# Kernel tuning notes

Hardware: AMD Instinct MI355X
Metric: run time of the kernel (lower is better)

Reference implementation:

```python
import jax, jax.numpy as jnp
import numpy as np

B, T, D, H, QK = 4, 2048, 1024, 16, 64
MAX_WAVELENGTH = 10000


def apply_rope(x, positions):
    # x: [B, T, H, d]; positions: [B, T] int
    d = x.shape[-1]
    fraction = 2 * jnp.arange(0, d // 2, dtype=jnp.int32) / d
    timescale = MAX_WAVELENGTH ** fraction  # [d/2]
    sinusoid = positions[..., None] / timescale[None, :]  # [B, T, d/2]
    sinusoid = sinusoid[..., None, :]  # [B, T, 1, d/2]
    sin, cos = jnp.sin(sinusoid), jnp.cos(sinusoid)
    x1, x2 = jnp.split(x, 2, axis=-1)
    return jnp.concatenate([x1 * cos - x2 * sin, x2 * cos + x1 * sin], axis=-1).astype(x.dtype)


def rms_norm(x, scale):
    var = jnp.mean(jnp.square(x), axis=-1, keepdims=True)
    return x * jax.lax.rsqrt(var + 1e-6) * (1 + scale)


def setup_inputs() -> dict:
    key = jax.random.key(0)
    ks = jax.random.split(key, 12)
    s = 0.02
    pos = jnp.broadcast_to(jnp.arange(T, dtype=jnp.int32), (B, T))
    causal = jnp.tril(jnp.ones((T, T), dtype=bool))[None, None]  # [1,1,T,T]
    return {
        "q": jax.random.normal(ks[0], (B, T, D), jnp.float32),
        "kv": jax.random.normal(ks[1], (B, T, D), jnp.float32),
        "mask": jnp.broadcast_to(causal, (B, 1, T, T)),
        "q_positions": pos,
        "kv_positions": pos,
        "Wq": jax.random.normal(ks[2], (D, H * QK), jnp.float32) * s,
        "bq": jnp.zeros((H * QK,), jnp.float32),
        "Wk": jax.random.normal(ks[3], (D, H * QK), jnp.float32) * s,
        "bk": jnp.zeros((H * QK,), jnp.float32),
        "Wv": jax.random.normal(ks[4], (D, H * QK), jnp.float32) * s,
        "bv": jnp.zeros((H * QK,), jnp.float32),
        "q_scale": jnp.zeros((QK,), jnp.float32),
        "k_scale": jnp.zeros((QK,), jnp.float32),
        "head_scale": jnp.zeros((1, H, 1), jnp.float32),
        "Wo": jax.random.normal(ks[5], (H * QK, D), jnp.float32) * s,
        "bo": jnp.zeros((D,), jnp.float32),
    }


def reference(q, kv, mask, q_positions, kv_positions, Wq, bq, Wk, bk, Wv, bv,
              q_scale, k_scale, head_scale, Wo, bo):
    qh = (q @ Wq + bq).reshape(B, T, H, QK)
    kh = (kv @ Wk + bk).reshape(B, T, H, QK)
    vh = (kv @ Wv + bv).reshape(B, T, H, QK)
    # qk layer norm (RMSNorm with (1+scale))
    qh = rms_norm(qh, q_scale)
    kh = rms_norm(kh, k_scale)
    # RoPE
    qh = apply_rope(qh, q_positions)
    kh = apply_rope(kh, kv_positions)
    # attention
    logits = jnp.einsum('bthd,bThd->bhtT', qh, kh) / np.sqrt(QK).astype(q.dtype)
    logits = jnp.where(mask, logits, jnp.finfo(logits.dtype).min)
    weights = jax.nn.softmax(logits, axis=-1)
    weights = jnp.where(mask, weights, 0)
    attn = jnp.einsum('bhtT,bThd->bthd', weights, vh)
    attn = attn * (1 + head_scale)  # [1,H,1] broadcasts over (t,h,d)
    return attn.reshape(B, T, H * QK) @ Wo + bo
```

## Files before the change

### kernel.cpp

```cpp
#include <hip/hip_runtime.h>
#include <math.h>

#define BB 4
#define TT 2048
#define DD 1024
#define HH 16
#define QKD 64
#define MM (BB*TT)
#define NN 1024
#define KK 1024

typedef unsigned short u16;
typedef __attribute__((ext_vector_type(8))) short short8;
typedef __attribute__((ext_vector_type(4))) float float4v;

__device__ __forceinline__ u16 f2bf(float f) {
    union { float f; unsigned u; } v; v.f = f;
    unsigned r = (v.u + 0x7FFFu + ((v.u >> 16) & 1u)) >> 16;
    return (u16)r;
}

typedef __attribute__((address_space(3))) unsigned lds_u32_t;
typedef __attribute__((address_space(1))) const unsigned glb_u32_t;
__device__ __forceinline__ void gl2lds16(const u16* g, u16* l) {
    __builtin_amdgcn_global_load_lds((glb_u32_t*)g, (lds_u32_t*)l, 16, 0, 0);
}

__global__ __launch_bounds__(256) void acast_kernel(
    const float* __restrict__ a, const float* __restrict__ b,
    u16* __restrict__ da, u16* __restrict__ db)
{
    const float* s = blockIdx.y ? b : a;
    u16* d = blockIdx.y ? db : da;
    size_t i = ((size_t)blockIdx.x * 256 + threadIdx.x) * 4;
    float4 v = *(const float4*)&s[i];
    ushort4 o = { f2bf(v.x), f2bf(v.y), f2bf(v.z), f2bf(v.w) };
    *(ushort4*)&d[i] = o;
}

__global__ __launch_bounds__(256) void wt_kernel(
    const float* __restrict__ Wq, const float* __restrict__ Wk,
    const float* __restrict__ Wv, const float* __restrict__ Wo,
    u16* __restrict__ dstbase)
{
    const int z = blockIdx.z;
    const float* src = (z == 0) ? Wq : (z == 1) ? Wk : (z == 2) ? Wv : Wo;
    u16* out = dstbase + (size_t)z * (KK * NN);
    const int bi = blockIdx.y, bj = blockIdx.x;
    __shared__ float tile[64][65];
    const int t = threadIdx.x;
    #pragma unroll
    for (int p = 0; p < 4; p++) {
        int idx = p * 256 + t;
        int r = idx >> 4, c4 = (idx & 15) << 2;
        float4 v = *(const float4*)&src[(size_t)(bi * 64 + r) * NN + bj * 64 + c4];
        tile[r][c4 + 0] = v.x; tile[r][c4 + 1] = v.y;
        tile[r][c4 + 2] = v.z; tile[r][c4 + 3] = v.w;
    }
    __syncthreads();
    #pragma unroll
    for (int p = 0; p < 4; p++) {
        int idx = p * 256 + t;
        int rn = idx >> 4, c4 = (idx & 15) << 2;
        ushort4 o = { f2bf(tile[c4 + 0][rn]), f2bf(tile[c4 + 1][rn]),
                      f2bf(tile[c4 + 2][rn]), f2bf(tile[c4 + 3][rn]) };
        *(ushort4*)&out[(size_t)(bj * 64 + rn) * KK + bi * 64 + c4] = o;
    }
}

__device__ __forceinline__ void gemm_mainloop(
    const u16* __restrict__ A, const u16* __restrict__ Bt,
    int m0, int n0, u16* As, u16* Bs, float4v (&acc)[4][4])
{
    const int tid = threadIdx.x;
    const int wave = tid >> 6, lane = tid & 63;
    const int l15 = lane & 15, lg = lane >> 4;
    const int wm = wave >> 1, wn = wave & 1;

    const int lr = lane >> 3;
    const int lc = lane & 7;

    for (int k0 = 0; k0 < KK; k0 += 64) {
        #pragma unroll
        for (int i = 0; i < 4; i++) {
            int chunk = wave * 4 + i;
            int row = chunk * 8 + lr;
            int gcb = lc ^ (row & 7);
            gl2lds16(A  + (size_t)(m0 + row) * KK + k0 + gcb * 8, As + chunk * 512);
            gl2lds16(Bt + (size_t)(n0 + row) * KK + k0 + gcb * 8, Bs + chunk * 512);
        }
        __syncthreads();

        short8 af[2][4], bf[2][4];
        #pragma unroll
        for (int kc = 0; kc < 2; kc++) {
            #pragma unroll
            for (int x = 0; x < 4; x++) {
                int ra = wm * 64 + x * 16 + l15;
                int sa = (kc * 4 + lg) ^ (ra & 7);
                af[kc][x] = *(const short8*)(As + ra * 64 + sa * 8);
                int rb = wn * 64 + x * 16 + l15;
                int sb = (kc * 4 + lg) ^ (rb & 7);
                bf[kc][x] = *(const short8*)(Bs + rb * 64 + sb * 8);
            }
        }
        #pragma unroll
        for (int mi = 0; mi < 4; mi++)
            #pragma unroll
            for (int nj = 0; nj < 4; nj++) {
                acc[mi][nj] = __builtin_amdgcn_mfma_f32_16x16x32_bf16(af[0][mi], bf[0][nj], acc[mi][nj], 0, 0, 0);
                acc[mi][nj] = __builtin_amdgcn_mfma_f32_16x16x32_bf16(af[1][mi], bf[1][nj], acc[mi][nj], 0, 0, 0);
            }
        __syncthreads();
    }
}

__global__ __launch_bounds__(256) void qkv_gemm(
    const u16* __restrict__ qb, const u16* __restrict__ kvb,
    const u16* __restrict__ Wt,
    const float* __restrict__ bq, const float* __restrict__ bk, const float* __restrict__ bv,
    const int* __restrict__ qpos, const int* __restrict__ kpos,
    const float* __restrict__ q_scale, const float* __restrict__ k_scale,
    u16* __restrict__ qh, u16* __restrict__ kh, u16* __restrict__ vh)
{
    __shared__ u16 As[128 * 64];
    __shared__ u16 Bs[128 * 64];

    const int z = blockIdx.z;
    const u16* A        = (z == 0) ? qb : kvb;
    const u16* B        = Wt + (size_t)z * (KK * NN);
    const float* bias   = (z == 0) ? bq : (z == 1) ? bk : bv;
    const float* scl    = (z == 0) ? q_scale : k_scale;
    const int* pos_arr  = (z == 0) ? qpos : kpos;
    u16* dst            = (z == 0) ? qh : (z == 1) ? kh : vh;

    const int m0 = blockIdx.y * 128, n0 = blockIdx.x * 128;

    float4v acc[4][4];
    #pragma unroll
    for (int i = 0; i < 4; i++)
        #pragma unroll
        for (int j = 0; j < 4; j++) acc[i][j] = (float4v){0.f, 0.f, 0.f, 0.f};

    gemm_mainloop(A, B, m0, n0, As, Bs, acc);

    const int lane = threadIdx.x & 63, wave = threadIdx.x >> 6;
    const int l15 = lane & 15, lg = lane >> 4;
    const int wm = wave >> 1, wn = wave & 1;
    const int mbase = m0 + wm * 64;
    const int nbase = n0 + wn * 64;
    const int h = nbase >> 6;

    float bia[4], sc[4];
    #pragma unroll
    for (int nj = 0; nj < 4; nj++) {
        bia[nj] = bias[nbase - (h << 6) + h * 64 + nj * 16 + l15];
        sc[nj]  = 1.0f + scl[nj * 16 + l15];
    }
    float invts[2];
    #pragma unroll
    for (int p = 0; p < 2; p++)
        invts[p] = powf(10000.0f, -(float)(p * 16 + l15) * (1.0f / 32.0f));

    const float QMUL = 0.125f * 1.44269504088896340736f;

    #pragma unroll
    for (int mi = 0; mi < 4; mi++) {
        #pragma unroll
        for (int r = 0; r < 4; r++) {
            const int m = mbase + mi * 16 + lg * 4 + r;
            const int b = m >> 11, t = m & 2047;
            float v[4];
            #pragma unroll
            for (int nj = 0; nj < 4; nj++) v[nj] = acc[mi][nj][r] + bia[nj];

            if (z < 2) {
                float ss = v[0]*v[0] + v[1]*v[1] + v[2]*v[2] + v[3]*v[3];
                ss += __shfl_xor(ss, 1);
                ss += __shfl_xor(ss, 2);
                ss += __shfl_xor(ss, 4);
                ss += __shfl_xor(ss, 8);
                float rn = rsqrtf(ss * (1.0f / 64.0f) + 1e-6f);
                #pragma unroll
                for (int nj = 0; nj < 4; nj++) v[nj] = v[nj] * rn * sc[nj];

                const float pos = (float)pos_arr[b * TT + t];
                #pragma unroll
                for (int p = 0; p < 2; p++) {
                    float ang = pos * invts[p];
                    float s = sinf(ang), c = cosf(ang);
                    float x1 = v[p], x2 = v[p + 2];
                    v[p]     = x1 * c - x2 * s;
                    v[p + 2] = x2 * c + x1 * s;
                }
                if (z == 0) {
                    #pragma unroll
                    for (int nj = 0; nj < 4; nj++) v[nj] *= QMUL;
                }
            }
            u16* op = dst + ((size_t)((b * HH + h) * TT + t)) * QKD + l15;
            #pragma unroll
            for (int nj = 0; nj < 4; nj++) op[nj * 16] = f2bf(v[nj]);
        }
    }
}

__global__ __launch_bounds__(256) void out_gemm(
    const u16* __restrict__ A, const u16* __restrict__ Bt,
    const float* __restrict__ bo, float* __restrict__ out)
{
    __shared__ u16 As[128 * 64];
    __shared__ u16 Bs[128 * 64];

    const int m0 = blockIdx.y * 128, n0 = blockIdx.x * 128;

    float4v acc[4][4];
    #pragma unroll
    for (int i = 0; i < 4; i++)
        #pragma unroll
        for (int j = 0; j < 4; j++) acc[i][j] = (float4v){0.f, 0.f, 0.f, 0.f};

    gemm_mainloop(A, Bt, m0, n0, As, Bs, acc);

    const int lane = threadIdx.x & 63, wave = threadIdx.x >> 6;
    const int l15 = lane & 15, lg = lane >> 4;
    const int wm = wave >> 1, wn = wave & 1;
    const int mbase = m0 + wm * 64;
    const int nbase = n0 + wn * 64;

    float bov[4];
    #pragma unroll
    for (int nj = 0; nj < 4; nj++) bov[nj] = bo[nbase + nj * 16 + l15];

    #pragma unroll
    for (int mi = 0; mi < 4; mi++)
        #pragma unroll
        for (int r = 0; r < 4; r++) {
            const int m = mbase + mi * 16 + lg * 4 + r;
            float* op = out + (size_t)m * NN + nbase + l15;
            #pragma unroll
            for (int nj = 0; nj < 4; nj++)
                op[nj * 16] = acc[mi][nj][r] + bov[nj];
        }
}

#define LSTR 72

__global__ __launch_bounds__(256) void attn_mfma(
    const u16* __restrict__ qh, const u16* __restrict__ kh,
    const u16* __restrict__ vh, const float* __restrict__ head_scale,
    u16* __restrict__ out)
{
    __shared__ u16 Ks[64 * LSTR];
    __shared__ u16 Vt[64 * LSTR];
    __shared__ u16 Ps[4][16 * LSTR];

    const int b = blockIdx.z, h = blockIdx.y, qt = blockIdx.x;
    const int t0 = qt * 64;
    const int tid  = threadIdx.x;
    const int wave = tid >> 6, lane = tid & 63;
    const int l15 = lane & 15, lg = lane >> 4;

    const size_t bh_off = (size_t)(b * HH + h) * TT * QKD;
    const u16* qbh = qh + bh_off;
    const u16* kbh = kh + bh_off;
    const u16* vbh = vh + bh_off;

    short8 qfrag[2];
    #pragma unroll
    for (int kc = 0; kc < 2; kc++)
        qfrag[kc] = *(const short8*)(qbh + (size_t)(t0 + wave * 16 + l15) * QKD
                                      + kc * 32 + lg * 8);

    float4v o_acc[4];
    #pragma unroll
    for (int nt = 0; nt < 4; nt++) o_acc[nt] = (float4v){0.f, 0.f, 0.f, 0.f};
    float m_run[4] = {-INFINITY, -INFINITY, -INFINITY, -INFINITY};
    float l_run[4] = {0.f, 0.f, 0.f, 0.f};

    for (int j0 = 0; j0 <= t0; j0 += 64) {
        #pragma unroll
        for (int r = 0; r < 2; r++) {
            int idx = r * 256 + tid;
            int row = idx >> 3, cb = (idx & 7) * 8;
            short8 k8 = *(const short8*)(kbh + (size_t)(j0 + row) * QKD + cb);
            *(short8*)&Ks[row * LSTR + cb] = k8;

            int j   = tid & 63;
            int dv0 = (tid >> 6) * 8 + r * 32;
            short8 v8 = *(const short8*)(vbh + (size_t)(j0 + j) * QKD + dv0);
            #pragma unroll
            for (int i = 0; i < 8; i++)
                Vt[(dv0 + i) * LSTR + j] = (u16)v8[i];
        }
        __syncthreads();

        float4v sarr[4];
        #pragma unroll
        for (int nt = 0; nt < 4; nt++) {
            float4v s = (float4v){0.f, 0.f, 0.f, 0.f};
            #pragma unroll
            for (int kc = 0; kc < 2; kc++) {
                short8 bfrag = *(const short8*)&Ks[(nt * 16 + l15) * LSTR + kc * 32 + lg * 8];
                s = __builtin_amdgcn_mfma_f32_16x16x32_bf16(qfrag[kc], bfrag, s, 0, 0, 0);
            }
            sarr[nt] = s;
        }

        const int qbase = t0 + wave * 16 + lg * 4;
        if (j0 == t0) {
            #pragma unroll
            for (int nt = 0; nt < 4; nt++) {
                int jkey = j0 + nt * 16 + l15;
                #pragma unroll
                for (int r = 0; r < 4; r++)
                    if (jkey > qbase + r) sarr[nt][r] = -INFINITY;
            }
        }

        float alpha[4], rowsum[4];
        #pragma unroll
        for (int r = 0; r < 4; r++) {
            float m = fmaxf(fmaxf(sarr[0][r], sarr[1][r]), fmaxf(sarr[2][r], sarr[3][r]));
            m = fmaxf(m, __shfl_xor(m, 1));
            m = fmaxf(m, __shfl_xor(m, 2));
            m = fmaxf(m, __shfl_xor(m, 4));
            m = fmaxf(m, __shfl_xor(m, 8));
            float m_new = fmaxf(m_run[r], m);
            alpha[r] = exp2f(m_run[r] - m_new);
            m_run[r] = m_new;
            rowsum[r] = 0.f;
        }
        u16* pw = Ps[wave];
        #pragma unroll
        for (int nt = 0; nt < 4; nt++) {
            #pragma unroll
            for (int r = 0; r < 4; r++) {
                float p = exp2f(sarr[nt][r] - m_run[r]);
                rowsum[r] += p;
                pw[(lg * 4 + r) * LSTR + nt * 16 + l15] = f2bf(p);
            }
        }
        #pragma unroll
        for (int r = 0; r < 4; r++) {
            float rs = rowsum[r];
            rs += __shfl_xor(rs, 1);
            rs += __shfl_xor(rs, 2);
            rs += __shfl_xor(rs, 4);
            rs += __shfl_xor(rs, 8);
            l_run[r] = l_run[r] * alpha[r] + rs;
        }
        #pragma unroll
        for (int nt = 0; nt < 4; nt++)
            #pragma unroll
            for (int r = 0; r < 4; r++)
                o_acc[nt][r] *= alpha[r];

        short8 pf[2];
        #pragma unroll
        for (int kc = 0; kc < 2; kc++)
            pf[kc] = *(const short8*)&pw[l15 * LSTR + kc * 32 + lg * 8];
        #pragma unroll
        for (int nt = 0; nt < 4; nt++) {
            #pragma unroll
            for (int kc = 0; kc < 2; kc++) {
                short8 vfrag = *(const short8*)&Vt[(nt * 16 + l15) * LSTR + kc * 32 + lg * 8];
                o_acc[nt] = __builtin_amdgcn_mfma_f32_16x16x32_bf16(pf[kc], vfrag, o_acc[nt], 0, 0, 0);
            }
        }
        __syncthreads();
    }

    const float hs = 1.0f + head_scale[h];
    #pragma unroll
    for (int r = 0; r < 4; r++) {
        const int q = t0 + wave * 16 + lg * 4 + r;
        const float f = hs / l_run[r];
        u16* op = out + ((size_t)(b * TT + q) * NN) + h * QKD + l15;
        #pragma unroll
        for (int nt = 0; nt < 4; nt++)
            op[nt * 16] = f2bf(o_acc[nt][r] * f);
    }
}

extern "C" void kernel_launch(void* const* d_in, const int* in_sizes, int n_in,
                              void* d_out, int out_size, void* d_ws, size_t ws_size,
                              hipStream_t stream)
{
    const float* q          = (const float*)d_in[0];
    const float* kv         = (const float*)d_in[1];
    const int*   qpos       = (const int*)d_in[3];
    const int*   kpos       = (const int*)d_in[4];
    const float* Wq         = (const float*)d_in[5];
    const float* bq         = (const float*)d_in[6];
    const float* Wk         = (const float*)d_in[7];
    const float* bk         = (const float*)d_in[8];
    const float* Wv         = (const float*)d_in[9];
    const float* bv         = (const float*)d_in[10];
    const float* q_scale    = (const float*)d_in[11];
    const float* k_scale    = (const float*)d_in[12];
    const float* head_scale = (const float*)d_in[13];
    const float* Wo         = (const float*)d_in[14];
    const float* bo         = (const float*)d_in[15];
    float* out = (float*)d_out;

    char* ws = (char*)d_ws;
    u16* qb     = (u16*)(ws);
    u16* kvb    = (u16*)(ws + (16u << 20));
    u16* Wt     = (u16*)(ws + (32u << 20));
    u16* qh_b   = (u16*)(ws + (40u << 20));
    u16* kh_b   = (u16*)(ws + (56u << 20));
    u16* vh_b   = (u16*)(ws + (72u << 20));
    u16* attn_b = (u16*)(ws + (88u << 20));

    acast_kernel<<<dim3(MM * DD / (256 * 4), 2), 256, 0, stream>>>(q, kv, qb, kvb);
    wt_kernel<<<dim3(16, 16, 4), 256, 0, stream>>>(Wq, Wk, Wv, Wo, Wt);
    qkv_gemm<<<dim3(NN / 128, MM / 128, 3), 256, 0, stream>>>(
        qb, kvb, Wt, bq, bk, bv, qpos, kpos, q_scale, k_scale, qh_b, kh_b, vh_b);
    attn_mfma<<<dim3(TT / 64, HH, BB), 256, 0, stream>>>(qh_b, kh_b, vh_b, head_scale, attn_b);
    out_gemm<<<dim3(NN / 128, MM / 128), 256, 0, stream>>>(attn_b, Wt + (size_t)3 * KK * NN, bo, out);
}
```

Measured before the change: 528.6 us.

## Double-buffer attention K/V via async LDS loads with pre-transposed V

```diff
diff --git a/kernel.cpp b/kernel.cpp
--- a/kernel.cpp
+++ b/kernel.cpp
@@ -20,6 +20,12 @@
     return (u16)r;
 }
 
+__device__ __forceinline__ unsigned cvt_pk_bf16(float lo, float hi) {
+    unsigned r;
+    asm("v_cvt_pk_bf16_f32 %0, %1, %2" : "=v"(r) : "v"(lo), "v"(hi));
+    return r;
+}
+
 typedef __attribute__((address_space(3))) unsigned lds_u32_t;
 typedef __attribute__((address_space(1))) const unsigned glb_u32_t;
 __device__ __forceinline__ void gl2lds16(const u16* g, u16* l) {
@@ -121,7 +127,7 @@
     const float* __restrict__ bq, const float* __restrict__ bk, const float* __restrict__ bv,
     const int* __restrict__ qpos, const int* __restrict__ kpos,
     const float* __restrict__ q_scale, const float* __restrict__ k_scale,
-    u16* __restrict__ qh, u16* __restrict__ kh, u16* __restrict__ vh)
+    u16* __restrict__ qh, u16* __restrict__ kh, u16* __restrict__ vt)
 {
     __shared__ u16 As[128 * 64];
     __shared__ u16 Bs[128 * 64];
@@ -132,7 +138,7 @@
     const float* bias   = (z == 0) ? bq : (z == 1) ? bk : bv;
     const float* scl    = (z == 0) ? q_scale : k_scale;
     const int* pos_arr  = (z == 0) ? qpos : kpos;
-    u16* dst            = (z == 0) ? qh : (z == 1) ? kh : vh;
+    u16* dst            = (z == 0) ? qh : (z == 1) ? kh : vt;
 
     const int m0 = blockIdx.y * 128, n0 = blockIdx.x * 128;
 
@@ -197,10 +203,14 @@
                     #pragma unroll
                     for (int nj = 0; nj < 4; nj++) v[nj] *= QMUL;
                 }
-            }
-            u16* op = dst + ((size_t)((b * HH + h) * TT + t)) * QKD + l15;
-            #pragma unroll
-            for (int nj = 0; nj < 4; nj++) op[nj * 16] = f2bf(v[nj]);
+                u16* op = dst + ((size_t)((b * HH + h) * TT + t)) * QKD + l15;
+                #pragma unroll
+                for (int nj = 0; nj < 4; nj++) op[nj * 16] = f2bf(v[nj]);
+            } else {
+                u16* op = dst + ((size_t)((b * HH + h) * QKD) + l15) * TT + t;
+                #pragma unroll
+                for (int nj = 0; nj < 4; nj++) op[(size_t)(nj * 16) * TT] = f2bf(v[nj]);
+            }
         }
     }
 }
@@ -244,27 +254,26 @@
         }
 }
 
-#define LSTR 72
-
 __global__ __launch_bounds__(256) void attn_mfma(
     const u16* __restrict__ qh, const u16* __restrict__ kh,
-    const u16* __restrict__ vh, const float* __restrict__ head_scale,
+    const u16* __restrict__ vt, const float* __restrict__ head_scale,
     u16* __restrict__ out)
 {
-    __shared__ u16 Ks[64 * LSTR];
-    __shared__ u16 Vt[64 * LSTR];
-    __shared__ u16 Ps[4][16 * LSTR];
+    __shared__ __align__(16) u16 Ks[2][64 * 64];
+    __shared__ __align__(16) u16 Vs[2][64 * 64];
+    __shared__ __align__(16) u16 Ps[4][16 * 64];
 
     const int b = blockIdx.z, h = blockIdx.y, qt = blockIdx.x;
     const int t0 = qt * 64;
     const int tid  = threadIdx.x;
     const int wave = tid >> 6, lane = tid & 63;
     const int l15 = lane & 15, lg = lane >> 4;
-
-    const size_t bh_off = (size_t)(b * HH + h) * TT * QKD;
-    const u16* qbh = qh + bh_off;
-    const u16* kbh = kh + bh_off;
-    const u16* vbh = vh + bh_off;
+    const int l7 = l15 & 7;
+
+    const size_t bh = (size_t)(b * HH + h);
+    const u16* qbh  = qh + bh * TT * QKD;
+    const u16* kbh  = kh + bh * TT * QKD;
+    const u16* vtbh = vt + bh * QKD * TT;
 
     short8 qfrag[2];
     #pragma unroll
@@ -272,28 +281,33 @@
         qfrag[kc] = *(const short8*)(qbh + (size_t)(t0 + wave * 16 + l15) * QKD
                                       + kc * 32 + lg * 8);
 
+    auto stage = [&](int buf, int j0s) {
+        #pragma unroll
+        for (int rr = 0; rr < 2; rr++) {
+            const int c   = rr * 256 + tid;
+            const int row = c >> 3;
+            const int g   = (c & 7) ^ (row & 7);
+            u16* ldsK = &Ks[buf][(rr * 256 + (wave << 6)) * 8];
+            u16* ldsV = &Vs[buf][(rr * 256 + (wave << 6)) * 8];
+            gl2lds16(kbh  + (size_t)(j0s + row) * QKD + g * 8, ldsK);
+            gl2lds16(vtbh + (size_t)row * TT + j0s + g * 8, ldsV);
+        }
+    };
+
     float4v o_acc[4];
     #pragma unroll
     for (int nt = 0; nt < 4; nt++) o_acc[nt] = (float4v){0.f, 0.f, 0.f, 0.f};
     float m_run[4] = {-INFINITY, -INFINITY, -INFINITY, -INFINITY};
     float l_run[4] = {0.f, 0.f, 0.f, 0.f};
 
+    stage(0, 0);
+    __syncthreads();
+
+    const int qbase = t0 + wave * 16 + lg * 4;
+
     for (int j0 = 0; j0 <= t0; j0 += 64) {
-        #pragma unroll
-        for (int r = 0; r < 2; r++) {
-            int idx = r * 256 + tid;
-            int row = idx >> 3, cb = (idx & 7) * 8;
-            short8 k8 = *(const short8*)(kbh + (size_t)(j0 + row) * QKD + cb);
-            *(short8*)&Ks[row * LSTR + cb] = k8;
-
-            int j   = tid & 63;
-            int dv0 = (tid >> 6) * 8 + r * 32;
-            short8 v8 = *(const short8*)(vbh + (size_t)(j0 + j) * QKD + dv0);
-            #pragma unroll
-            for (int i = 0; i < 8; i++)
-                Vt[(dv0 + i) * LSTR + j] = (u16)v8[i];
-        }
-        __syncthreads();
+        const int cur = (j0 >> 6) & 1;
+        if (j0 + 64 <= t0) stage(cur ^ 1, j0 + 64);
 
         float4v sarr[4];
         #pragma unroll
@@ -301,13 +315,13 @@
             float4v s = (float4v){0.f, 0.f, 0.f, 0.f};
             #pragma unroll
             for (int kc = 0; kc < 2; kc++) {
-                short8 bfrag = *(const short8*)&Ks[(nt * 16 + l15) * LSTR + kc * 32 + lg * 8];
+                const short8 bfrag = *(const short8*)
+                    &Ks[cur][(nt * 16 + l15) * 64 + ((kc * 4 + lg) ^ l7) * 8];
                 s = __builtin_amdgcn_mfma_f32_16x16x32_bf16(qfrag[kc], bfrag, s, 0, 0, 0);
             }
             sarr[nt] = s;
         }
 
-        const int qbase = t0 + wave * 16 + lg * 4;
         if (j0 == t0) {
             #pragma unroll
             for (int nt = 0; nt < 4; nt++) {
@@ -318,7 +332,7 @@
             }
         }
 
-        float alpha[4], rowsum[4];
+        float pm[4];
         #pragma unroll
         for (int r = 0; r < 4; r++) {
             float m = fmaxf(fmaxf(sarr[0][r], sarr[1][r]), fmaxf(sarr[2][r], sarr[3][r]));
@@ -326,45 +340,54 @@
             m = fmaxf(m, __shfl_xor(m, 2));
             m = fmaxf(m, __shfl_xor(m, 4));
             m = fmaxf(m, __shfl_xor(m, 8));
-            float m_new = fmaxf(m_run[r], m);
-            alpha[r] = exp2f(m_run[r] - m_new);
-            m_run[r] = m_new;
-            rowsum[r] = 0.f;
-        }
+            pm[r] = m;
+        }
+        float grow = fmaxf(fmaxf(pm[0] - m_run[0], pm[1] - m_run[1]),
+                           fmaxf(pm[2] - m_run[2], pm[3] - m_run[3]));
+        if (__any(grow > 8.0f)) {
+            #pragma unroll
+            for (int r = 0; r < 4; r++) {
+                float mn = fmaxf(m_run[r], pm[r]);
+                float a  = exp2f(m_run[r] - mn);
+                m_run[r] = mn;
+                l_run[r] *= a;
+                #pragma unroll
+                for (int nt = 0; nt < 4; nt++) o_acc[nt][r] *= a;
+            }
+        }
+
         u16* pw = Ps[wave];
+        float lp[4] = {0.f, 0.f, 0.f, 0.f};
         #pragma unroll
         for (int nt = 0; nt < 4; nt++) {
-            #pragma unroll
-            for (int r = 0; r < 4; r++) {
-                float p = exp2f(sarr[nt][r] - m_run[r]);
-                rowsum[r] += p;
-                pw[(lg * 4 + r) * LSTR + nt * 16 + l15] = f2bf(p);
-            }
-        }
-        #pragma unroll
-        for (int r = 0; r < 4; r++) {
-            float rs = rowsum[r];
-            rs += __shfl_xor(rs, 1);
-            rs += __shfl_xor(rs, 2);
-            rs += __shfl_xor(rs, 4);
-            rs += __shfl_xor(rs, 8);
-            l_run[r] = l_run[r] * alpha[r] + rs;
-        }
-        #pragma unroll
-        for (int nt = 0; nt < 4; nt++)
-            #pragma unroll
-            for (int r = 0; r < 4; r++)
-                o_acc[nt][r] *= alpha[r];
+            float p0 = exp2f(sarr[nt][0] - m_run[0]);
+            float p1 = exp2f(sarr[nt][1] - m_run[1]);
+            float p2 = exp2f(sarr[nt][2] - m_run[2]);
+            float p3 = exp2f(sarr[nt][3] - m_run[3]);
+            lp[0] += p0; lp[1] += p1; lp[2] += p2; lp[3] += p3;
+            unsigned wlo = cvt_pk_bf16(p0, p1);
+            unsigned whi = cvt_pk_bf16(p2, p3);
+            const int gb = nt * 2 + (l15 >> 3);
+            const int r0 = lg * 4;
+            pw[(r0 + 0) * 64 + ((gb ^ ((r0 + 0) & 7))) * 8 + l7] = (u16)wlo;
+            pw[(r0 + 1) * 64 + ((gb ^ ((r0 + 1) & 7))) * 8 + l7] = (u16)(wlo >> 16);
+            pw[(r0 + 2) * 64 + ((gb ^ ((r0 + 2) & 7))) * 8 + l7] = (u16)whi;
+            pw[(r0 + 3) * 64 + ((gb ^ ((r0 + 3) & 7))) * 8 + l7] = (u16)(whi >> 16);
+        }
+        #pragma unroll
+        for (int r = 0; r < 4; r++) l_run[r] += lp[r];
 
         short8 pf[2];
         #pragma unroll
         for (int kc = 0; kc < 2; kc++)
-            pf[kc] = *(const short8*)&pw[l15 * LSTR + kc * 32 + lg * 8];
+            pf[kc] = *(const short8*)&pw[l15 * 64 + ((kc * 4 + lg) ^ l7) * 8];
+
         #pragma unroll
         for (int nt = 0; nt < 4; nt++) {
             #pragma unroll
             for (int kc = 0; kc < 2; kc++) {
-                short8 vfrag = *(const short8*)&Vt[(nt * 16 + l15) * LSTR + kc * 32 + lg * 8];
+                const short8 vfrag = *(const short8*)
+                    &Vs[cur][(nt * 16 + l15) * 64 + ((kc * 4 + lg) ^ l7) * 8];
                 o_acc[nt] = __builtin_amdgcn_mfma_f32_16x16x32_bf16(pf[kc], vfrag, o_acc[nt], 0, 0, 0);
             }
         }
@@ -374,8 +397,13 @@
     const float hs = 1.0f + head_scale[h];
     #pragma unroll
     for (int r = 0; r < 4; r++) {
+        float l = l_run[r];
+        l += __shfl_xor(l, 1);
+        l += __shfl_xor(l, 2);
+        l += __shfl_xor(l, 4);
+        l += __shfl_xor(l, 8);
         const int q = t0 + wave * 16 + lg * 4 + r;
-        const float f = hs / l_run[r];
+        const float f = hs / l;
         u16* op = out + ((size_t)(b * TT + q) * NN) + h * QKD + l15;
         #pragma unroll
         for (int nt = 0; nt < 4; nt++)
@@ -410,13 +438,13 @@
     u16* Wt     = (u16*)(ws + (32u << 20));
     u16* qh_b   = (u16*)(ws + (40u << 20));
     u16* kh_b   = (u16*)(ws + (56u << 20));
-    u16* vh_b   = (u16*)(ws + (72u << 20));
+    u16* vt_b   = (u16*)(ws + (72u << 20));
     u16* attn_b = (u16*)(ws + (88u << 20));
 
     acast_kernel<<<dim3(MM * DD / (256 * 4), 2), 256, 0, stream>>>(q, kv, qb, kvb);
     wt_kernel<<<dim3(16, 16, 4), 256, 0, stream>>>(Wq, Wk, Wv, Wo, Wt);
     qkv_gemm<<<dim3(NN / 128, MM / 128, 3), 256, 0, stream>>>(
-        qb, kvb, Wt, bq, bk, bv, qpos, kpos, q_scale, k_scale, qh_b, kh_b, vh_b);
-    attn_mfma<<<dim3(TT / 64, HH, BB), 256, 0, stream>>>(qh_b, kh_b, vh_b, head_scale, attn_b);
+        qb, kvb, Wt, bq, bk, bv, qpos, kpos, q_scale, k_scale, qh_b, kh_b, vt_b);
+    attn_mfma<<<dim3(TT / 64, HH, BB), 256, 0, stream>>>(qh_b, kh_b, vt_b, head_scale, attn_b);
     out_gemm<<<dim3(NN / 128, MM / 128), 256, 0, stream>>>(attn_b, Wt + (size_t)3 * KK * NN, bo, out);
 }
```

Measured after the change: 707.1 us. 33.8% more time.
